# Optimization experiments

Measured on AMD Instinct MI355X. Metric: run time of the kernel, lower is better.

## Reference

```python
import jax, jax.numpy as jnp
import numpy as np

N, E, D_IN, D_OUT, MAX_DEG = 50000, 800000, 128, 128, 64
ALPHA = 0.5


def _linear_params(key, fan_in, fan_out):
    s = 1.0 / np.sqrt(fan_in)
    kw, kb = jax.random.split(key)
    W = jax.random.uniform(kw, (fan_out, fan_in), jnp.float32, -s, s)
    b = jax.random.uniform(kb, (fan_out,), jnp.float32, -s, s)
    return W, b


def setup_inputs() -> dict:
    key = jax.random.key(0)
    ks = jax.random.split(key, 16)
    x = jax.random.normal(ks[0], (N, D_IN), jnp.float32)
    edge_index = jax.random.randint(ks[1], (2, E), 0, N, dtype=jnp.int64)
    in_degree = jax.random.randint(ks[2], (N,), 0, MAX_DEG, dtype=jnp.int64)
    out_degree = jax.random.randint(ks[3], (N,), 0, MAX_DEG, dtype=jnp.int64)
    out_deg_mask = jax.random.uniform(ks[4], (N,), jnp.float32)
    out_deg_mask_bias = jax.random.uniform(ks[5], (N,), jnp.float32)
    in_deg_mask = jax.random.uniform(ks[6], (N,), jnp.float32)
    in_deg_mask_bias = jax.random.uniform(ks[7], (N,), jnp.float32)
    W_src, b_src = _linear_params(ks[8], D_IN, D_OUT)
    W_dst, b_dst = _linear_params(ks[9], D_IN, D_OUT)
    W_out_f, b_out_f = _linear_params(ks[10], D_IN, 1)
    W_in_f, b_in_f = _linear_params(ks[11], D_IN, 1)
    W_fc, b_fc = _linear_params(ks[12], D_IN, D_OUT)
    # degree embedding tables, padding_idx=0 -> row 0 zeroed
    in_deg_table = (jax.random.normal(ks[13], (MAX_DEG, D_IN), jnp.float32)).at[0].set(0.0)
    out_deg_table = (jax.random.normal(ks[14], (MAX_DEG, D_IN), jnp.float32)).at[0].set(0.0)
    return {
        "x": x, "edge_index": edge_index,
        "in_degree": in_degree, "out_degree": out_degree,
        "out_deg_mask": out_deg_mask, "out_deg_mask_bias": out_deg_mask_bias,
        "in_deg_mask": in_deg_mask, "in_deg_mask_bias": in_deg_mask_bias,
        "W_src": W_src, "b_src": b_src, "W_dst": W_dst, "b_dst": b_dst,
        "W_out_f": W_out_f, "b_out_f": b_out_f, "W_in_f": W_in_f, "b_in_f": b_in_f,
        "W_fc": W_fc, "b_fc": b_fc,
        "in_deg_table": in_deg_table, "out_deg_table": out_deg_table,
    }


def reference(x, edge_index, in_degree, out_degree,
              out_deg_mask, out_deg_mask_bias, in_deg_mask, in_deg_mask_bias,
              W_src, b_src, W_dst, b_dst,
              W_out_f, b_out_f, W_in_f, b_in_f,
              W_fc, b_fc, in_deg_table, out_deg_table):
    n = x.shape[0]
    row, col = edge_index[0], edge_index[1]
    ones = jnp.ones(row.shape[0], x.dtype)
    # directed norm D_out^{-1/2} A D_in^{-1/2}; transpose reuses the same edge weights
    out_deg = jax.ops.segment_sum(ones, row, num_segments=n)
    in_deg = jax.ops.segment_sum(ones, col, num_segments=n)
    o_inv = jnp.where(out_deg > 0, jax.lax.rsqrt(jnp.maximum(out_deg, 1e-12)), 0.0)
    i_inv = jnp.where(in_deg > 0, jax.lax.rsqrt(jnp.maximum(in_deg, 1e-12)), 0.0)
    w = o_inv[row] * i_inv[col]  # [E]
    # adj_norm @ x and adj_t_norm @ x (SpMM via gather + segment_sum)
    out_nei = jax.ops.segment_sum(w[:, None] * x[col], row, num_segments=n)  # [N,D]
    in_nei = jax.ops.segment_sum(w[:, None] * x[row], col, num_segments=n)   # [N,D]
    # degree-gated filter
    c_out = (out_nei - x + out_deg_table[out_degree]) @ W_out_f.T + b_out_f  # [N,1]
    c_in = (in_nei - x + in_deg_table[in_degree]) @ W_in_f.T + b_in_f        # [N,1]
    C = jax.nn.softmax(jnp.concatenate([c_out, c_in], axis=1), axis=1)        # tau_softmax, tau=1
    C_out = C[:, 0:1] * out_deg_mask[:, None] + out_deg_mask_bias[:, None]
    C_in = C[:, 1:2] * in_deg_mask[:, None] + in_deg_mask_bias[:, None]
    out = (C_out * (out_nei @ W_src.T + b_src)
           + C_in * (in_nei @ W_dst.T + b_dst)
           + ALPHA * (x @ W_fc.T + b_fc))
    return out, C_in, C_out
```

## Files before the change

kernel.cpp:

```cpp
#include <hip/hip_runtime.h>

#define NN 50000
#define EE 800000
#define DD 128
#define CAP 48
#define MT 64
#define XSL 6250
#define PB 128
#define PCB (8 * PB)

typedef short short8_t __attribute__((ext_vector_type(8)));
typedef float f32x4 __attribute__((ext_vector_type(4)));
typedef float f32x2 __attribute__((ext_vector_type(2)));

__device__ __forceinline__ unsigned short f2bf(float f) {
    union { float f; unsigned int i; } v; v.f = f;
    unsigned int x = v.i;
    x += 0x7FFFu + ((x >> 16) & 1u);
    return (unsigned short)(x >> 16);
}
__device__ __forceinline__ unsigned int pack2(float a, float b) {
    return (unsigned int)f2bf(a) | ((unsigned int)f2bf(b) << 16);
}
__device__ __forceinline__ f32x2 bfup(unsigned int u) {
    union { unsigned int i; float f; } lo, hi;
    lo.i = u << 16;
    hi.i = u & 0xFFFF0000u;
    f32x2 r; r.x = lo.f; r.y = hi.f;
    return r;
}
__device__ __forceinline__ void pkfma(f32x2& a, f32x2 b, f32x2 w) {
    asm("v_pk_fma_f32 %0, %1, %2, %0" : "+v"(a) : "v"(b), "v"(w));
}
__device__ __forceinline__ void accw(f32x2* ac, uint4 u, float w) {
    f32x2 wp; wp.x = w; wp.y = w;
    pkfma(ac[0], bfup(u.x), wp); pkfma(ac[1], bfup(u.y), wp);
    pkfma(ac[2], bfup(u.z), wp); pkfma(ac[3], bfup(u.w), wp);
}

__global__ void __launch_bounds__(256) k_pc(
    const int* __restrict__ ei, int* __restrict__ cnt,
    unsigned short* __restrict__ bkt_row, unsigned short* __restrict__ bkt_col,
    const float* __restrict__ x,
    const float* __restrict__ W_src, const float* __restrict__ W_dst,
    const float* __restrict__ W_fc,
    unsigned short* __restrict__ xb, unsigned short* __restrict__ wbf)
{
    if (blockIdx.x < PCB) {
        int xcd = blockIdx.x & 7;
        int b   = blockIdx.x >> 3;
        int lo = xcd * XSL, hi = lo + XSL;
        for (int e = b * 256 + threadIdx.x; e < EE; e += PB * 256) {
            int r = ei[e];
            int c = ei[EE + e];
            if (r >= lo && r < hi) {
                int po = atomicAdd(&cnt[r], 1);
                if (po < CAP) bkt_row[(size_t)r * CAP + po] = (unsigned short)c;
            }
            if (c >= lo && c < hi) {
                int pi = atomicAdd(&cnt[NN + c], 1);
                if (pi < CAP) bkt_col[(size_t)c * CAP + pi] = (unsigned short)r;
            }
        }
    } else {
        int t = (blockIdx.x - PCB) * 256 + threadIdx.x;
        int base = t * 4;
        if (base < NN * DD) {
            float4 v = *(const float4*)(x + base);
            uint2 p; p.x = pack2(v.x, v.y); p.y = pack2(v.z, v.w);
            *(uint2*)(xb + base) = p;
        } else {
            int b2 = base - NN * DD;
            if (b2 < 3 * 16384) {
                int src = b2 >> 14;
                int off = b2 & 16383;
                const float* W = (src == 0) ? W_src : (src == 1) ? W_dst : W_fc;
                float sc = (src == 2) ? 0.5f : 1.0f;
                float4 v = *(const float4*)(W + off);
                uint2 p; p.x = pack2(v.x * sc, v.y * sc); p.y = pack2(v.z * sc, v.w * sc);
                *(uint2*)(wbf + b2) = p;
            }
        }
    }
}

__global__ void __launch_bounds__(256) k_gather(
    const uint4* __restrict__ xb4, const float4* __restrict__ x4,
    const unsigned short* __restrict__ bkt_row, const unsigned short* __restrict__ bkt_col,
    const int* __restrict__ cnt,
    const int* __restrict__ in_degree, const int* __restrict__ out_degree,
    const float* __restrict__ odm, const float* __restrict__ odmb,
    const float* __restrict__ idm, const float* __restrict__ idmb,
    const float4* __restrict__ W_out_f4, const float* __restrict__ b_out_f,
    const float4* __restrict__ W_in_f4, const float* __restrict__ b_in_f,
    const float4* __restrict__ in_tab4, const float4* __restrict__ out_tab4,
    uint2* __restrict__ onb2, uint2* __restrict__ inb2,
    float* __restrict__ scbuf,
    float* __restrict__ outCin, float* __restrict__ outCout)
{
    __shared__ float4 sred[2][4][2][16][3];
    __shared__ float sg[2][2];
    __shared__ float sC[2][2];
    int half = threadIdx.x >> 7;
    int n = blockIdx.x * 2 + half;
    int t = threadIdx.x & 127;
    int g = t >> 5;
    int l = t & 31;
    int dir = g >> 1;
    int gd  = g & 1;
    int sub = l >> 4;
    int li  = l & 15;
    int shamt = gd << 4;

    const unsigned short* bp = ((dir == 0) ? bkt_row : bkt_col) + (size_t)n * CAP;
    const int* wcnt = (dir == 0) ? (cnt + NN) : cnt;
    int rawdeg = cnt[dir * NN + n];
    int deg = (rawdeg > CAP) ? CAP : rawdeg;

    unsigned int bw = (l < 24) ? *(const unsigned int*)(bp + 2 * l) : 0u;

    float w_l = 0.0f;
    {
        unsigned int pr = __shfl(bw, l >> 1, 32);
        int il = (pr >> ((l & 1) << 4)) & 0xffff;
        if (l < deg) w_l = 1.0f / sqrtf((float)wcnt[il]);
    }

    f32x2 ac[4];
    ac[0] = (f32x2)0.0f; ac[1] = (f32x2)0.0f; ac[2] = (f32x2)0.0f; ac[3] = (f32x2)0.0f;

    if (deg <= 32) {
        int j = gd;
        for (; j + 14 < deg; j += 16) {
            int s0 = j + 2 * sub, s1 = s0 + 4, s2 = s0 + 8, s3 = s0 + 12;
            int i0 = (__shfl(bw, s0 >> 1, 32) >> shamt) & 0xffff;
            int i1 = (__shfl(bw, s1 >> 1, 32) >> shamt) & 0xffff;
            int i2 = (__shfl(bw, s2 >> 1, 32) >> shamt) & 0xffff;
            int i3 = (__shfl(bw, s3 >> 1, 32) >> shamt) & 0xffff;
            uint4 u0 = xb4[(size_t)i0 * 16 + li];
            uint4 u1 = xb4[(size_t)i1 * 16 + li];
            uint4 u2 = xb4[(size_t)i2 * 16 + li];
            uint4 u3 = xb4[(size_t)i3 * 16 + li];
            float w0 = __shfl(w_l, s0, 32);
            float w1 = __shfl(w_l, s1, 32);
            float w2v = __shfl(w_l, s2, 32);
            float w3 = __shfl(w_l, s3, 32);
            accw(ac, u0, w0); accw(ac, u1, w1); accw(ac, u2, w2v); accw(ac, u3, w3);
        }
        for (; j + 6 < deg; j += 8) {
            int s0 = j + 2 * sub, s1 = s0 + 4;
            int i0 = (__shfl(bw, s0 >> 1, 32) >> shamt) & 0xffff;
            int i1 = (__shfl(bw, s1 >> 1, 32) >> shamt) & 0xffff;
            uint4 u0 = xb4[(size_t)i0 * 16 + li];
            uint4 u1 = xb4[(size_t)i1 * 16 + li];
            float w0 = __shfl(w_l, s0, 32);
            float w1 = __shfl(w_l, s1, 32);
            accw(ac, u0, w0); accw(ac, u1, w1);
        }
        for (; j < deg; j += 4) {
            int s0 = j + 2 * sub;
            int sc = (s0 < deg) ? s0 : gd;
            int i0 = (__shfl(bw, sc >> 1, 32) >> shamt) & 0xffff;
            float w0 = __shfl(w_l, sc, 32);
            if (s0 < deg) {
                uint4 u0 = xb4[(size_t)i0 * 16 + li];
                accw(ac, u0, w0);
            }
        }
    } else {
        for (int j = gd; j < deg; j += 4) {
            int s0 = j + 2 * sub;
            int sc = (s0 < deg) ? s0 : gd;
            int i0 = (__shfl(bw, sc >> 1, 32) >> shamt) & 0xffff;
            if (s0 < deg) {
                float w0 = 1.0f / sqrtf((float)wcnt[i0]);
                uint4 u0 = xb4[(size_t)i0 * 16 + li];
                accw(ac, u0, w0);
            }
        }
    }

    sred[half][g][sub][li][0] = make_float4(ac[0].x, ac[0].y, ac[1].x, ac[1].y);
    sred[half][g][sub][li][1] = make_float4(ac[2].x, ac[2].y, ac[3].x, ac[3].y);
    __syncthreads();

    float4 r = make_float4(0.f, 0.f, 0.f, 0.f);
    if (gd == 0) {
        int src = l >> 1, q = l & 1;
        int g0 = dir * 2;
        float4 b0 = sred[half][g0][0][src][q];
        float4 b1 = sred[half][g0][1][src][q];
        float4 b2 = sred[half][g0 + 1][0][src][q];
        float4 b3 = sred[half][g0 + 1][1][src][q];
        float wn = (rawdeg > 0) ? (1.0f / sqrtf((float)rawdeg)) : 0.0f;
        r.x = wn * (b0.x + b1.x + b2.x + b3.x);
        r.y = wn * (b0.y + b1.y + b2.y + b3.y);
        r.z = wn * (b0.z + b1.z + b2.z + b3.z);
        r.w = wn * (b0.w + b1.w + b2.w + b3.w);
        float4 xv = x4[(size_t)n * 32 + l];
        float4 tb, wf;
        if (dir == 0) {
            int odg = out_degree[n];
            odg = (odg < 0) ? 0 : (odg > 63 ? 63 : odg);
            tb = out_tab4[(size_t)odg * 32 + l];
            wf = W_out_f4[l];
        } else {
            int idg = in_degree[n];
            idg = (idg < 0) ? 0 : (idg > 63 ? 63 : idg);
            tb = in_tab4[(size_t)idg * 32 + l];
            wf = W_in_f4[l];
        }
        float pv = (r.x - xv.x + tb.x) * wf.x + (r.y - xv.y + tb.y) * wf.y
                 + (r.z - xv.z + tb.z) * wf.z + (r.w - xv.w + tb.w) * wf.w;
        #pragma unroll
        for (int off = 16; off > 0; off >>= 1) pv += __shfl_down(pv, off);
        if (l == 0) sg[half][dir] = pv;
    }
    __syncthreads();
    if (t == 0) {
        float c_out = sg[half][0] + b_out_f[0];
        float c_in  = sg[half][1] + b_in_f[0];
        float m  = fmaxf(c_out, c_in);
        float eo = expf(c_out - m);
        float e2 = expf(c_in  - m);
        float inv = 1.0f / (eo + e2);
        float Cout = (eo * inv) * odm[n] + odmb[n];
        float Cin  = (e2 * inv) * idm[n] + idmb[n];
        sC[half][0] = Cout; sC[half][1] = Cin;
        scbuf[2 * n]     = Cout;
        scbuf[2 * n + 1] = Cin;
        outCout[n] = Cout;
        outCin[n]  = Cin;
    }
    __syncthreads();
    if (gd == 0) {
        float C = sC[half][dir];
        uint2 pw; pw.x = pack2(C * r.x, C * r.y); pw.y = pack2(C * r.z, C * r.w);
        ((dir == 0) ? onb2 : inb2)[(size_t)n * 32 + l] = pw;
    }
}

__global__ void __launch_bounds__(256) k_gemm(
    const unsigned int* __restrict__ xb32,
    const unsigned int* __restrict__ onb32, const unsigned int* __restrict__ inb32,
    const unsigned short* __restrict__ wbf,
    const float* __restrict__ b_src, const float* __restrict__ b_dst,
    const float* __restrict__ b_fc,
    const float* __restrict__ scbuf,
    float* __restrict__ out)
{
    __shared__ unsigned short sA[MT * 72];
    __shared__ unsigned short sBt[DD * 72];

    int tid = threadIdx.x;
    int wid = tid >> 6;
    int lane = tid & 63;
    int ml = lane & 15;
    int kq = lane >> 4;
    int n0 = blockIdx.x * MT;

    f32x4 accv[8];
    #pragma unroll
    for (int i = 0; i < 8; i++) accv[i] = (f32x4)0.0f;

    const unsigned int* srcs[3] = { onb32, inb32, xb32 };

    uint4 pa0, pa1, pb0, pb1, pb2, pb3;

    auto load_chunk = [&](int kt, uint4& a0, uint4& a1,
                          uint4& b0, uint4& b1, uint4& b2, uint4& b3) {
        int srcsel = kt >> 1;
        int k0 = (kt & 1) * 64;
        const unsigned int* S = srcs[srcsel];
        {
            int s = tid;
            int gn = n0 + (s >> 3);
            a0 = make_uint4(0u, 0u, 0u, 0u);
            if (gn < NN) a0 = *(const uint4*)(S + (size_t)gn * 64 + (k0 >> 1) + (s & 7) * 4);
        }
        {
            int s = tid + 256;
            int gn = n0 + (s >> 3);
            a1 = make_uint4(0u, 0u, 0u, 0u);
            if (gn < NN) a1 = *(const uint4*)(S + (size_t)gn * 64 + (k0 >> 1) + (s & 7) * 4);
        }
        const unsigned short* W = wbf + srcsel * 16384 + k0;
        b0 = *(const uint4*)(W + ((tid) >> 3) * DD + ((tid) & 7) * 8);
        b1 = *(const uint4*)(W + ((tid + 256) >> 3) * DD + ((tid + 256) & 7) * 8);
        b2 = *(const uint4*)(W + ((tid + 512) >> 3) * DD + ((tid + 512) & 7) * 8);
        b3 = *(const uint4*)(W + ((tid + 768) >> 3) * DD + ((tid + 768) & 7) * 8);
    };

    load_chunk(0, pa0, pa1, pb0, pb1, pb2, pb3);

    for (int kt = 0; kt < 6; kt++) {
        *(uint4*)(sA + (tid >> 3) * 72 + (tid & 7) * 8) = pa0;
        *(uint4*)(sA + ((tid + 256) >> 3) * 72 + ((tid + 256) & 7) * 8) = pa1;
        *(uint4*)(sBt + (tid >> 3) * 72 + (tid & 7) * 8) = pb0;
        *(uint4*)(sBt + ((tid + 256) >> 3) * 72 + ((tid + 256) & 7) * 8) = pb1;
        *(uint4*)(sBt + ((tid + 512) >> 3) * 72 + ((tid + 512) & 7) * 8) = pb2;
        *(uint4*)(sBt + ((tid + 768) >> 3) * 72 + ((tid + 768) & 7) * 8) = pb3;
        __syncthreads();

        if (kt < 5) load_chunk(kt + 1, pa0, pa1, pb0, pb1, pb2, pb3);

        #pragma unroll
        for (int ks = 0; ks < 64; ks += 32) {
            short8_t a = *(const short8_t*)(sA + (16 * wid + ml) * 72 + ks + kq * 8);
            #pragma unroll
            for (int i = 0; i < 8; i++) {
                short8_t b = *(const short8_t*)(sBt + (16 * i + ml) * 72 + ks + kq * 8);
                accv[i] = __builtin_amdgcn_mfma_f32_16x16x32_bf16(a, b, accv[i], 0, 0, 0);
            }
        }
        __syncthreads();
    }

    int row_base = n0 + 16 * wid + 4 * kq;
    #pragma unroll
    for (int r = 0; r < 4; r++) {
        int row = row_base + r;
        if (row >= NN) continue;
        float Cout = scbuf[2 * row];
        float Cin  = scbuf[2 * row + 1];
        #pragma unroll
        for (int i = 0; i < 8; i++) {
            int col = 16 * i + ml;
            out[(size_t)row * DD + col] =
                accv[i][r] + Cout * b_src[col] + Cin * b_dst[col] + 0.5f * b_fc[col];
        }
    }
}

extern "C" void kernel_launch(void* const* d_in, const int* in_sizes, int n_in,
                              void* d_out, int out_size, void* d_ws, size_t ws_size,
                              hipStream_t stream) {
    const float* x    = (const float*)d_in[0];
    const int* ei     = (const int*)d_in[1];
    const int* in_degree  = (const int*)d_in[2];
    const int* out_degree = (const int*)d_in[3];
    const float* odm  = (const float*)d_in[4];
    const float* odmb = (const float*)d_in[5];
    const float* idm  = (const float*)d_in[6];
    const float* idmb = (const float*)d_in[7];
    const float* W_src = (const float*)d_in[8];
    const float* b_src = (const float*)d_in[9];
    const float* W_dst = (const float*)d_in[10];
    const float* b_dst = (const float*)d_in[11];
    const float* W_out_f = (const float*)d_in[12];
    const float* b_out_f = (const float*)d_in[13];
    const float* W_in_f  = (const float*)d_in[14];
    const float* b_in_f  = (const float*)d_in[15];
    const float* W_fc    = (const float*)d_in[16];
    const float* b_fc    = (const float*)d_in[17];
    const float* in_tab  = (const float*)d_in[18];
    const float* out_tab = (const float*)d_in[19];

    unsigned short* xb  = (unsigned short*)d_ws;
    unsigned short* onb = xb + (size_t)NN * DD;
    unsigned short* inb = onb + (size_t)NN * DD;
    float* scbuf = (float*)(inb + (size_t)NN * DD);
    unsigned short* wbf = (unsigned short*)(scbuf + 2 * NN);
    int* cnt     = (int*)(wbf + 3 * 16384);
    unsigned short* bkt_row = (unsigned short*)(cnt + 2 * NN);
    unsigned short* bkt_col = bkt_row + (size_t)NN * CAP;

    hipMemsetAsync(cnt, 0, (size_t)2 * NN * sizeof(int), stream);

    int conv_quads = (NN * DD + 3 * 16384) / 4;
    int conv_blocks = (conv_quads + 255) / 256;
    k_pc<<<PCB + conv_blocks, 256, 0, stream>>>(ei, cnt, bkt_row, bkt_col,
                                                x, W_src, W_dst, W_fc, xb, wbf);

    float* out_p  = (float*)d_out;
    float* cin_p  = out_p + (size_t)NN * DD;
    float* cout_p = cin_p + NN;

    k_gather<<<NN / 2, 256, 0, stream>>>((const uint4*)xb, (const float4*)x,
                                         bkt_row, bkt_col, cnt,
                                         in_degree, out_degree,
                                         odm, odmb, idm, idmb,
                                         (const float4*)W_out_f, b_out_f,
                                         (const float4*)W_in_f, b_in_f,
                                         (const float4*)in_tab, (const float4*)out_tab,
                                         (uint2*)onb, (uint2*)inb,
                                         scbuf, cin_p, cout_p);

    k_gemm<<<(NN + MT - 1) / MT, 256, 0, stream>>>(
        (const unsigned int*)xb, (const unsigned int*)onb, (const unsigned int*)inb,
        wbf, b_src, b_dst, b_fc, scbuf, out_p);
}
```

Baseline: 267.2 us.

## Bucket edges with LDS-local histogram and batched global slot reservation

The edge-bucketing phase moves from one global atomic per edge per direction to 64 blocks, each owning one node slice, one direction and one quarter of the edges. Each block builds a per-node histogram in shared memory, reserves contiguous slots with a single global atomicAdd per nonzero node, then scatters payloads using local atomic decrements. This is meant to cut global atomic traffic and contention. In exchange, only 64 blocks with about 50KB of LDS each do the bucketing, so it has much less parallelism and each block reads its edge chunk twice.

Measured after the change: 857.4 us. 3.21x slower.

```diff
diff --git a/kernel.cpp b/kernel.cpp
--- a/kernel.cpp
+++ b/kernel.cpp
@@ -6,8 +6,8 @@
 #define CAP 48
 #define MT 64
 #define XSL 6250
-#define PB 128
-#define PCB (8 * PB)
+#define APCB 64
+#define ECHUNK (EE / 4)
 
 typedef short short8_t __attribute__((ext_vector_type(8)));
 typedef float f32x4 __attribute__((ext_vector_type(4)));
@@ -46,24 +46,42 @@
     const float* __restrict__ W_fc,
     unsigned short* __restrict__ xb, unsigned short* __restrict__ wbf)
 {
-    if (blockIdx.x < PCB) {
-        int xcd = blockIdx.x & 7;
-        int b   = blockIdx.x >> 3;
-        int lo = xcd * XSL, hi = lo + XSL;
-        for (int e = b * 256 + threadIdx.x; e < EE; e += PB * 256) {
-            int r = ei[e];
-            int c = ei[EE + e];
-            if (r >= lo && r < hi) {
-                int po = atomicAdd(&cnt[r], 1);
-                if (po < CAP) bkt_row[(size_t)r * CAP + po] = (unsigned short)c;
+    if (blockIdx.x < APCB) {
+        __shared__ unsigned int lcnt[XSL];
+        __shared__ unsigned int lbase[XSL];
+        int xcd  = blockIdx.x & 7;
+        int setb = blockIdx.x >> 3;
+        int dirc = setb & 1;
+        int chnk = setb >> 1;
+        int lo = xcd * XSL;
+        const int* key = ei + (dirc ? EE : 0);
+        const int* pay = ei + (dirc ? 0 : EE);
+        int e0 = chnk * ECHUNK, e1 = e0 + ECHUNK;
+        int* gc = cnt + dirc * NN;
+        unsigned short* bkt = dirc ? bkt_col : bkt_row;
+
+        for (int i = threadIdx.x; i < XSL; i += 256) lcnt[i] = 0u;
+        __syncthreads();
+        for (int e = e0 + threadIdx.x; e < e1; e += 256) {
+            int k = key[e] - lo;
+            if ((unsigned)k < (unsigned)XSL) atomicAdd(&lcnt[k], 1u);
+        }
+        __syncthreads();
+        for (int i = threadIdx.x; i < XSL; i += 256) {
+            unsigned int c = lcnt[i];
+            lbase[i] = c ? (unsigned int)atomicAdd(&gc[lo + i], (int)c) : 0u;
+        }
+        __syncthreads();
+        for (int e = e0 + threadIdx.x; e < e1; e += 256) {
+            int k = key[e] - lo;
+            if ((unsigned)k < (unsigned)XSL) {
+                unsigned int lslot = atomicSub(&lcnt[k], 1u) - 1u;
+                unsigned int slot = lbase[k] + lslot;
+                if (slot < CAP) bkt[(size_t)(lo + k) * CAP + slot] = (unsigned short)pay[e];
             }
-            if (c >= lo && c < hi) {
-                int pi = atomicAdd(&cnt[NN + c], 1);
-                if (pi < CAP) bkt_col[(size_t)c * CAP + pi] = (unsigned short)r;
-            }
         }
     } else {
-        int t = (blockIdx.x - PCB) * 256 + threadIdx.x;
+        int t = (blockIdx.x - APCB) * 256 + threadIdx.x;
         int base = t * 4;
         if (base < NN * DD) {
             float4 v = *(const float4*)(x + base);
@@ -369,8 +387,8 @@
 
     int conv_quads = (NN * DD + 3 * 16384) / 4;
     int conv_blocks = (conv_quads + 255) / 256;
-    k_pc<<<PCB + conv_blocks, 256, 0, stream>>>(ei, cnt, bkt_row, bkt_col,
-                                                x, W_src, W_dst, W_fc, xb, wbf);
+    k_pc<<<APCB + conv_blocks, 256, 0, stream>>>(ei, cnt, bkt_row, bkt_col,
+                                                 x, W_src, W_dst, W_fc, xb, wbf);
 
     float* out_p  = (float*)d_out;
     float* cin_p  = out_p + (size_t)NN * DD;
```
